# Kernel tuning notes

Measured on AMD Instinct MI355X. Metric: run time of the kernel, lower is better.

The kernel has to match this reference:

```python
import jax, jax.numpy as jnp
import numpy as np

IN_CH, OUT_CH, K = 2, 16, 3
VLAYERS = 2
STRIDE, PAD, DIL = 1, 0, 1
B, L = 16, 1024
NQ = IN_CH * K          # 6 qubits per patch
DIM = 2 ** NQ           # 64-dim statevector

# basis bit table, qubit 0 = most significant axis
_bits = ((np.arange(DIM)[:, None] >> (NQ - 1 - np.arange(NQ)[None, :])) & 1).astype(np.float32)
_pairs = [(i, (i + 1) % NQ) for i in range(NQ)]  # CZ entangling ring
_cz = sum(_bits[:, i] * _bits[:, j] for i, j in _pairs)
CZ_SIGN = jnp.asarray(np.where(_cz.astype(np.int64) % 2 == 1, -1.0, 1.0).astype(np.float32))
Z_ALL = jnp.asarray(np.where(_bits.sum(1).astype(np.int64) % 2 == 1, -1.0, 1.0).astype(np.float32))
ENC = jnp.asarray(_bits - 0.5)  # RZ(x) diagonal exponents, [DIM, NQ]


def _apply_ry(state, theta, q):
    # state: [M, DIM] complex64, theta: [M] float32, RY on qubit q
    M = state.shape[0]
    s = state.reshape(M, 2 ** q, 2, 2 ** (NQ - 1 - q))
    c = jnp.cos(theta * 0.5)[:, None, None]
    sn = jnp.sin(theta * 0.5)[:, None, None]
    a0, a1 = s[:, :, 0, :], s[:, :, 1, :]
    return jnp.stack([c * a0 - sn * a1, sn * a0 + c * a1], axis=2).reshape(M, DIM)


def _forward(x, weight):
    Bn, C, Ln = x.shape
    L_out = (Ln + 2 * PAD - DIL * (K - 1) - 1) // STRIDE + 1
    xp = jnp.pad(x, ((0, 0), (0, 0), (PAD, PAD)))
    idx = jnp.arange(L_out)[:, None] * STRIDE + jnp.arange(K)[None, :] * DIL  # [L_out, K]
    patches = xp[:, :, idx]                                        # [B, C, L_out, K]
    patches = patches.transpose(0, 2, 1, 3).reshape(Bn * L_out, NQ)  # torch Unfold order: c*K + j
    Np = Bn * L_out
    x_rep = jnp.broadcast_to(patches[None], (OUT_CH, Np, NQ)).reshape(OUT_CH * Np, NQ)
    th = jnp.broadcast_to(weight[:, None], (OUT_CH, Np, NQ, VLAYERS)).reshape(OUT_CH * Np, NQ, VLAYERS)
    # encoding: H on all qubits then per-qubit RZ(x_i) -> uniform amps with data phases
    inv_sqrt_dim = np.float32(1.0 / np.sqrt(DIM))
    state = (inv_sqrt_dim * jnp.exp(1j * (x_rep @ ENC.T))).astype(jnp.complex64)  # [M, DIM]
    for l in range(VLAYERS):
        for q in range(NQ):
            state = _apply_ry(state, th[:, q, l], q)
        state = state * CZ_SIGN
    probs = state.real ** 2 + state.imag ** 2
    exp_val = probs @ Z_ALL                                        # [M], energy <Z..Z>
    # replicate the original module's reshape/permute exactly ([O, Np] flat -> [B, L_out, O])
    out = exp_val.reshape(Bn, L_out, OUT_CH).transpose(0, 2, 1)
    return out


def setup_inputs() -> dict:
    key = jax.random.key(0)
    kx, kw = jax.random.split(key)
    x = jax.random.normal(kx, (B, IN_CH, L), dtype=jnp.float32)
    weight = jax.random.normal(kw, (OUT_CH, NQ, VLAYERS), dtype=jnp.float32)
    return {"x": x, "weight": weight}


def reference(x, weight):
    return _forward(x, weight)
```

## Files before the change

### kernel.cpp

```cpp
#include <hip/hip_runtime.h>


#define L_IN  1024
#define L_OUT 1022
#define NP    16352
#define NS    64

__global__ __launch_bounds__(256) void qconv_kernel(
    const float* __restrict__ x, const float* __restrict__ w,
    float* __restrict__ out)
{
    __shared__ float wtrig[16][6][4];
    __shared__ float T[NS * 16];

    const int tid = threadIdx.x;

    if (tid < 96) {
        const int oc = tid / 6, q = tid - oc * 6;
        const float th1 = w[(oc * 6 + q) * 2 + 0];
        const float th2 = w[(oc * 6 + q) * 2 + 1];
        float s1, c1, s2, c2;
        __sincosf(th1, &s1, &c1);
        __sincosf(th2, &s2, &c2);
        wtrig[oc][q][0] = c1; wtrig[oc][q][1] = s1;
        wtrig[oc][q][2] = c2; wtrig[oc][q][3] = s2;
    }
    __syncthreads();

    for (int i = tid; i < NS * 16; i += 256) {
        const int s = i >> 4, oc = i & 15;
        float prod = 1.f;
        int ess = 0, n1 = 0;
        #pragma unroll
        for (int q = 0; q < 6; ++q) {
            const int in  = (s >> q) & 1;
            const int nxt = (s >> ((q + 1) % 6)) & 1;
            const int prv = (s >> ((q + 5) % 6)) & 1;
            const int odd = (nxt + prv) & 1;
            const float c1 = wtrig[oc][q][0], s1 = wtrig[oc][q][1];
            const float c2 = wtrig[oc][q][2], s2 = wtrig[oc][q][3];
            const float f = in ? (odd ? -s2 : -s2 * c1)
                               : (odd ?  c2 : -c2 * s1);
            ess += in & nxt;
            n1  += in & odd;
            prod *= f;
        }
        if ((ess ^ (n1 >> 1)) & 1) prod = -prod;
        T[i] = prod;
    }
    __syncthreads();

    const int oc = tid & 15;
    const int p  = blockIdx.x * 16 + (tid >> 4);
    const int bi = p / L_OUT;
    const int li = p - bi * L_OUT;

    const float* xb = x + bi * (2 * L_IN) + li;
    float cx[6], sx[6];
    #pragma unroll
    for (int c = 0; c < 2; ++c) {
        #pragma unroll
        for (int k = 0; k < 3; ++k) {
            const float v = xb[c * L_IN + k];
            __sincosf(v, &sx[c * 3 + k], &cx[c * 3 + k]);
        }
    }

    float acc = 0.f;
    #pragma unroll
    for (int s = 0; s < NS; ++s) {
        float m = T[(s << 4) | oc];
        #pragma unroll
        for (int q = 0; q < 6; ++q) {
            const int in  = (s >> q) & 1;
            const int odd = (((s >> ((q + 1) % 6)) & 1) +
                             ((s >> ((q + 5) % 6)) & 1)) & 1;
            if (in)        m *= odd ? sx[q] : cx[q];
            else if (!odd) m *= cx[q];
        }
        acc += m;
    }

    out[oc * NP + (p & 15) * L_OUT + (p >> 4)] = acc;
}

extern "C" void kernel_launch(void* const* d_in, const int* in_sizes, int n_in,
                              void* d_out, int out_size, void* d_ws, size_t ws_size,
                              hipStream_t stream) {
    const float* x = (const float*)d_in[0];
    const float* w = (const float*)d_in[1];
    float* out = (float*)d_out;
    qconv_kernel<<<dim3(NP / 16), dim3(256), 0, stream>>>(x, w, out);
}
```

Measured before the change: 61.68 us.

## Share per-patch data product across eight output channels per thread

Each thread now handles one patch and eight output channels, not one patch and one channel. The 64 data-dependent products are computed once and reused across eight FMAs against the shared T table. This cuts the redundant sin/cos and product work by a factor of eight per output. In exchange the grid shrinks to 128 blocks, each recomputing the T table, and registers rise with eight accumulators.

```diff
diff --git a/kernel.cpp b/kernel.cpp
--- a/kernel.cpp
+++ b/kernel.cpp
@@ -50,8 +50,11 @@
     }
     __syncthreads();
 
-    const int oc = tid & 15;
-    const int p  = blockIdx.x * 16 + (tid >> 4);
+    const int gid  = blockIdx.x * 256 + tid;
+    const int p    = gid >> 1;
+    const int half = gid & 1;
+    if (p >= NP) return;
+
     const int bi = p / L_OUT;
     const int li = p - bi * L_OUT;
 
@@ -66,22 +69,30 @@
         }
     }
 
-    float acc = 0.f;
+    float acc[8];
+    #pragma unroll
+    for (int j = 0; j < 8; ++j) acc[j] = 0.f;
+
+    const float* Tb = T + half * 8;
     #pragma unroll
     for (int s = 0; s < NS; ++s) {
-        float m = T[(s << 4) | oc];
+        float m = 1.f;
         #pragma unroll
         for (int q = 0; q < 6; ++q) {
             const int in  = (s >> q) & 1;
-            const int odd = (((s >> ((q + 1) % 6)) & 1) +
-                             ((s >> ((q + 5) % 6)) & 1)) & 1;
-            if (in)        m *= odd ? sx[q] : cx[q];
-            else if (!odd) m *= cx[q];
+            const int odd = (((s >> ((q + 1) % 6)) ^ (s >> ((q + 5) % 6)))) & 1;
+            if (odd) { if (in) m *= sx[q]; }
+            else       m *= cx[q];
         }
-        acc += m;
+        #pragma unroll
+        for (int j = 0; j < 8; ++j)
+            acc[j] = fmaf(Tb[s * 16 + j], m, acc[j]);
     }
 
-    out[oc * NP + (p & 15) * L_OUT + (p >> 4)] = acc;
+    const int obase = (p & 15) * L_OUT + (p >> 4);
+    #pragma unroll
+    for (int j = 0; j < 8; ++j)
+        out[(half * 8 + j) * NP + obase] = acc[j];
 }
 
 extern "C" void kernel_launch(void* const* d_in, const int* in_sizes, int n_in,
@@ -90,5 +101,5 @@
     const float* x = (const float*)d_in[0];
     const float* w = (const float*)d_in[1];
     float* out = (float*)d_out;
-    qconv_kernel<<<dim3(NP / 16), dim3(256), 0, stream>>>(x, w, out);
+    qconv_kernel<<<dim3((2 * NP + 255) / 256), dim3(256), 0, stream>>>(x, w, out);
 }
```

Result: no change. 61.01 us (-1.1%).
